# Kernel optimization log

Hardware: AMD Instinct MI355X
Metric: run time of the kernel (lower is better)

## Reference

```python
import jax, jax.numpy as jnp
import numpy as np

B, L, C, S, W, R = 2, 32, 32, 64, 64, 32
MH = 32  # forcing MLP hidden


def _conv3d(x, w, b, pad_hw):
    # x: [B, Cin, L, S, W], w: [Cout, Cin, 1, kh, kw]
    y = jax.lax.conv_general_dilated(
        x, w, window_strides=(1, 1, 1),
        padding=[(0, 0), (pad_hw, pad_hw), (pad_hw, pad_hw)],
        dimension_numbers=('NCDHW', 'OIDHW', 'NCDHW'))
    return y + b[None, :, None, None, None]


def _forward(x, listT, params_log_base, dispersion_mod, fm_W1, fm_b1, fm_W2, fm_b2,
             forcing_scale, U_re, U_im, V_re, V_im, pW_re, pW_im, pb_re, pb_im,
             convr_w, convr_b, convi_w, convi_b, projc_w, projc_b, ln_w, ln_b):
    b, l, c, s, w = x.shape
    r = U_re.shape[-1]
    pad = s // 4
    dt = listT.reshape(b, l, 1, 1, 1)

    # FFT with mirror padding along S
    xp = jnp.pad(x, ((0, 0), (0, 0), (0, 0), (pad, pad), (0, 0)), mode='reflect')
    h = jnp.fft.fft2(xp.astype(jnp.complex64), axes=(-2, -1), norm='ortho')

    # complex channel projection
    proj_W = pW_re + 1j * pW_im
    h = jnp.einsum('blcsw,cd->bldsw', h, proj_W)
    h = h + (pb_re + 1j * pb_im)[None, None, :, None, None]

    # back to spatial, crop pad, re-FFT
    hs = jnp.fft.ifft2(h, axes=(-2, -1), norm='ortho')[..., pad:-pad, :]
    h = jnp.fft.fft2(hs, axes=(-2, -1), norm='ortho')

    U = U_re + 1j * U_im          # [C, S, R]
    V = V_re + 1j * V_im          # [C, W, R]
    # zq[b,l,c,r,q] = sum_{s,w} h * conj(U)[c,s,r] * V[c,w,q]
    zq = jnp.einsum('blcsw,csr,cwq->blcrq', h, jnp.conj(U), V)

    nu_base = jnp.exp(params_log_base[0] + dispersion_mod[0]).reshape(1, 1, c, r, 1)
    th_base = jnp.exp(params_log_base[1] + dispersion_mod[1]).reshape(1, 1, c, r, 1)

    # forcing modulation
    ctx = x.mean(axis=(-2, -1))                       # [B, L, C]
    inp = jnp.concatenate([ctx, dt.reshape(b, l, 1)], axis=-1)
    mid = jnp.tanh(inp @ fm_W1 + fm_b1)
    mod = (mid @ fm_W2 + fm_b2).reshape(b, l, c, r, 2)
    dnu = (forcing_scale * jnp.tanh(mod[..., 0]))[..., None]
    dth = (forcing_scale * jnp.tanh(mod[..., 1]))[..., None]

    nu_t = jnp.maximum(nu_base * dt + dnu, 1e-6)       # [B, L, C, R, 1]
    th_t = th_base * dt + dth
    lamb = jnp.exp(jax.lax.complex(-nu_t, th_t))       # complex [B, L, C, R, 1]

    gamma = jnp.sqrt(jnp.maximum(1.0 - jnp.exp(-2.0 * nu_t), 1e-12))
    x_in = zq * gamma.astype(zq.dtype)                 # [B, L, C, R, R]

    # parallel linear-recurrence scan: z_t = lamb_t * z_{t-1} + x_t
    def comb(a, bb):
        a1, x1 = a
        a2, x2 = bb
        return a1 * a2, a2 * x1 + x2
    _, z_out = jax.lax.associative_scan(comb, (lamb, x_in), axis=1)

    # reconstruct spectral field and inverse FFT
    h_rec = jnp.einsum('blcrq,cwq,csr->blcsw', z_out, jnp.conj(V), U)
    h_sp = jnp.fft.ifft2(h_rec, axes=(-2, -1), norm='ortho')

    xr = jnp.transpose(h_sp.real, (0, 2, 1, 3, 4))     # [B, C, L, S, W]
    xi = jnp.transpose(h_sp.imag, (0, 2, 1, 3, 4))
    hr = _conv3d(xr, convr_w, convr_b, 1)
    hi = _conv3d(xi, convi_w, convi_b, 1)
    hf = _conv3d(jnp.concatenate([hr, hi], axis=1), projc_w, projc_b, 0)
    hf = jnp.transpose(hf, (0, 2, 1, 3, 4))            # [B, L, C, S, W]

    # LayerNorm over [S, W]
    mu = hf.mean(axis=(-2, -1), keepdims=True)
    var = hf.var(axis=(-2, -1), keepdims=True)
    hf = (hf - mu) / jnp.sqrt(var + 1e-5) * ln_w + ln_b

    return x + hf


def setup_inputs() -> dict:
    key = jax.random.key(0)
    ks = jax.random.split(key, 20)
    f32 = jnp.float32
    x = jax.random.normal(ks[0], (B, L, C, S, W), dtype=f32)
    listT = jax.random.uniform(ks[1], (B, L), dtype=f32, minval=0.5, maxval=1.5)

    r_min, r_max = 0.8, 0.99
    u1 = jax.random.uniform(ks[2], (C, R), dtype=f32)
    u2 = jax.random.uniform(ks[3], (C, R), dtype=f32)
    nu_log = jnp.log(-0.5 * jnp.log(u1 * (r_max ** 2 - r_min ** 2) + r_min ** 2))
    theta_log = jnp.log(u2 * (2.0 * np.pi))
    params_log_base = jnp.stack([nu_log, theta_log], axis=0)
    dispersion_mod = jnp.zeros((2, C, R), dtype=f32)

    fm_W1 = jax.random.normal(ks[4], (C + 1, MH), dtype=f32) / np.sqrt(C + 1)
    fm_b1 = jnp.zeros((MH,), dtype=f32)
    fm_W2 = jax.random.normal(ks[5], (MH, C * R * 2), dtype=f32) / np.sqrt(MH)
    fm_b2 = jnp.zeros((C * R * 2,), dtype=f32)
    forcing_scale = jnp.float32(0.1)

    cplx_scale = 1.0 / np.sqrt(2.0)
    U_re = jax.random.normal(ks[6], (C, S, R), dtype=f32) * cplx_scale / np.sqrt(S)
    U_im = jax.random.normal(ks[7], (C, S, R), dtype=f32) * cplx_scale / np.sqrt(S)
    V_re = jax.random.normal(ks[8], (C, W, R), dtype=f32) * cplx_scale / np.sqrt(W)
    V_im = jax.random.normal(ks[9], (C, W, R), dtype=f32) * cplx_scale / np.sqrt(W)
    pW_re = jax.random.normal(ks[10], (C, C), dtype=f32) * cplx_scale / np.sqrt(C)
    pW_im = jax.random.normal(ks[11], (C, C), dtype=f32) * cplx_scale / np.sqrt(C)
    pb_re = jnp.zeros((C,), dtype=f32)
    pb_im = jnp.zeros((C,), dtype=f32)

    convr_w = jax.random.normal(ks[12], (C, C, 1, 3, 3), dtype=f32) * (1.0 / np.sqrt(C * 9))
    convr_b = jnp.zeros((C,), dtype=f32)
    convi_w = jax.random.normal(ks[13], (C, C, 1, 3, 3), dtype=f32) * (1.0 / np.sqrt(C * 9))
    convi_b = jnp.zeros((C,), dtype=f32)
    projc_w = jax.random.normal(ks[14], (C, 2 * C, 1, 1, 1), dtype=f32) * (1.0 / np.sqrt(2 * C))
    projc_b = jnp.zeros((C,), dtype=f32)

    ln_w = jnp.ones((S, W), dtype=f32)
    ln_b = jnp.zeros((S, W), dtype=f32)

    return dict(x=x, listT=listT, params_log_base=params_log_base,
                dispersion_mod=dispersion_mod, fm_W1=fm_W1, fm_b1=fm_b1,
                fm_W2=fm_W2, fm_b2=fm_b2, forcing_scale=forcing_scale,
                U_re=U_re, U_im=U_im, V_re=V_re, V_im=V_im,
                pW_re=pW_re, pW_im=pW_im, pb_re=pb_re, pb_im=pb_im,
                convr_w=convr_w, convr_b=convr_b, convi_w=convi_w, convi_b=convi_b,
                projc_w=projc_w, projc_b=projc_b, ln_w=ln_w, ln_b=ln_b)


def reference(x, listT, params_log_base, dispersion_mod, fm_W1, fm_b1, fm_W2, fm_b2,
              forcing_scale, U_re, U_im, V_re, V_im, pW_re, pW_im, pb_re, pb_im,
              convr_w, convr_b, convi_w, convi_b, projc_w, projc_b, ln_w, ln_b):
    return _forward(x, listT, params_log_base, dispersion_mod, fm_W1, fm_b1, fm_W2,
                    fm_b2, forcing_scale, U_re, U_im, V_re, V_im, pW_re, pW_im,
                    pb_re, pb_im, convr_w, convr_b, convi_w, convi_b, projc_w,
                    projc_b, ln_w, ln_b)
```

## Files before the change

kernel.cpp:

```cpp
#include <hip/hip_runtime.h>


typedef __attribute__((ext_vector_type(8))) short short8;
typedef __attribute__((ext_vector_type(4))) float floatx4;

__device__ __forceinline__ unsigned pack_bf16(float re, float im) {
  unsigned a = __float_as_uint(re), b = __float_as_uint(im);
  a = (a + 0x7FFFu + ((a >> 16) & 1u)) >> 16;
  b = (b + 0x7FFFu + ((b >> 16) & 1u)) >> 16;
  return a | (b << 16);
}

__global__ __launch_bounds__(256) void k_prep(
    const float* __restrict__ U_re, const float* __restrict__ U_im,
    const float* __restrict__ V_re, const float* __restrict__ V_im,
    const float* __restrict__ projc_w,
    const float* __restrict__ convr_w, const float* __restrict__ convi_w,
    const float* __restrict__ x,
    unsigned* __restrict__ zqA, unsigned* __restrict__ recA,
    unsigned* __restrict__ recB, unsigned* __restrict__ Wtb,
    float* __restrict__ ctx) {
  const int bid = blockIdx.x;
  const int tid = threadIdx.x;
  if (bid < 2048) {
    __shared__ float2 tw[64];
    if (tid < 64) {
      float sa, ca;
      sincosf((float)tid * 0.09817477042468103f, &sa, &ca);
      tw[tid] = make_float2(ca, sa);
    }
    __syncthreads();
    int gid = bid * 256 + tid;
    const float *Ar, *Ai;
    int knum, mode, variant;
    bool plus;
    unsigned* dst;
    int didx;
    if (gid < 262144) {
      int c = gid >> 13, mat = (gid >> 11) & 3, m = (gid >> 6) & 31,
          kw = gid & 63;
      knum = kw; mode = m;
      if (mat < 2) { Ar = V_re + c * 2048; Ai = V_im + c * 2048; plus = false; }
      else         { Ar = U_re + c * 2048; Ai = U_im + c * 2048; plus = true; }
      variant = mat; dst = zqA; didx = gid;
    } else {
      int rid = gid - 262144;
      int c = rid >> 13, sub = rid & 8191;
      int which = sub >> 11, mm = (sub >> 5) & 63, k2 = sub & 31;
      knum = mm; mode = k2;
      if (which < 2) {
        Ar = U_re + c * 2048; Ai = U_im + c * 2048; plus = true;
        variant = 4 + which; dst = recA;
        didx = ((c * 2 + which) * 64 + mm) * 32 + k2;
      } else {
        Ar = V_re + c * 2048; Ai = V_im + c * 2048; plus = false;
        variant = 4 + which; dst = recB;
        didx = ((c * 2 + which - 2) * 64 + mm) * 32 + k2;
      }
    }
    float sr = 0.f, si = 0.f;
    for (int n = 0; n < 64; ++n) {
      float2 w = tw[(knum * n) & 63];
      float ar = Ar[n * 32 + mode], ai = Ai[n * 32 + mode];
      if (plus) { sr += ar * w.x - ai * w.y; si += ar * w.y + ai * w.x; }
      else      { sr += ar * w.x + ai * w.y; si += ai * w.x - ar * w.y; }
    }
    sr *= 0.125f; si *= 0.125f;
    unsigned pv;
    switch (variant) {
      case 0: pv = pack_bf16(sr, -si); break;
      case 1: pv = pack_bf16(si, sr); break;
      case 2: pv = pack_bf16(sr, si); break;
      case 3: pv = pack_bf16(-si, sr); break;
      case 4: pv = pack_bf16(sr, -si); break;
      case 5: pv = pack_bf16(si, sr); break;
      case 6: pv = pack_bf16(sr, si); break;
      default: pv = pack_bf16(-si, sr); break;
    }
    dst[didx] = pv;
  } else if (bid < 2084) {
    int gid = (bid - 2048) * 256 + tid;
    if (gid < 9216) {
      int co = gid / 288;
      int r2 = gid - co * 288;
      int tap = r2 >> 5, ci = r2 & 31;
      float sr = 0.f, si = 0.f;
      for (int m = 0; m < 32; ++m) {
        sr += projc_w[co * 64 + m]      * convr_w[(m * 32 + ci) * 9 + tap];
        si += projc_w[co * 64 + 32 + m] * convi_w[(m * 32 + ci) * 9 + tap];
      }
      Wtb[gid] = pack_bf16(sr, si);
    }
  } else {
    int blc = bid - 2084;
    const float* p = x + (size_t)blc * 4096;
    float s = 0.f;
    for (int i = tid; i < 4096; i += 256) s += p[i];
    for (int o = 32; o > 0; o >>= 1) s += __shfl_down(s, o, 64);
    __shared__ float wsum[4];
    if ((tid & 63) == 0) wsum[tid >> 6] = s;
    __syncthreads();
    if (tid == 0)
      ctx[blc] = (wsum[0] + wsum[1] + wsum[2] + wsum[3]) * (1.f / 4096.f);
  }
}

__global__ __launch_bounds__(256) void k_mix_mlp(
    const float* __restrict__ x, const float* __restrict__ pWr,
    const float* __restrict__ pWi, unsigned* __restrict__ hs,
    const float* __restrict__ ctx, const float* __restrict__ listT,
    const float* __restrict__ plb, const float* __restrict__ dmod,
    const float* __restrict__ W1, const float* __restrict__ b1,
    const float* __restrict__ W2, const float* __restrict__ b2,
    const float* __restrict__ fscale,
    float2* __restrict__ lam, float* __restrict__ gam) {
  const int tid = threadIdx.x;
  if (blockIdx.x < 1024) {
    int bl = blockIdx.x >> 4;
    int p = ((blockIdx.x & 15) << 8) + tid;
    const float* xb = x + (size_t)bl * 32 * 4096 + p;
    float xv[32];
#pragma unroll
    for (int ci = 0; ci < 32; ++ci) xv[ci] = xb[ci * 4096];
    unsigned* ho = hs + (size_t)bl * 32 * 4096 + p;
    for (int d = 0; d < 32; ++d) {
      float ar = 0.f, ai = 0.f;
#pragma unroll
      for (int ci = 0; ci < 32; ++ci) {
        float xc = xv[ci];
        ar += xc * pWr[ci * 32 + d];
        ai += xc * pWi[ci * 32 + d];
      }
      ho[(size_t)d * 4096] = pack_bf16(ar, ai);
    }
  } else {
    int bl = blockIdx.x - 1024;
    float dt = listT[bl];
    __shared__ float mid_s[32];
    if (tid < 32) {
      float a = b1[tid];
      for (int j = 0; j < 32; ++j) a += ctx[bl * 32 + j] * W1[j * 32 + tid];
      a += dt * W1[1024 + tid];
      mid_s[tid] = tanhf(a);
    }
    __syncthreads();
    float fs = fscale[0];
#pragma unroll
    for (int u = 0; u < 4; ++u) {
      int cr = u * 256 + tid;
      int col = cr * 2;
      float m0 = b2[col], m1 = b2[col + 1];
      for (int h = 0; h < 32; ++h) {
        float mh = mid_s[h];
        float2 w2 = *(const float2*)&W2[h * 2048 + col];
        m0 += mh * w2.x;
        m1 += mh * w2.y;
      }
      float dnu = fs * tanhf(m0);
      float dth = fs * tanhf(m1);
      float nub = expf(plb[cr] + dmod[cr]);
      float thb = expf(plb[1024 + cr] + dmod[1024 + cr]);
      float nut = fmaxf(nub * dt + dnu, 1e-6f);
      float tht = thb * dt + dth;
      float e = expf(-nut);
      float sa, ca;
      sincosf(tht, &sa, &ca);
      float g = sqrtf(fmaxf(1.f - expf(-2.f * nut), 1e-12f));
      int o = bl * 1024 + cr;
      lam[o] = make_float2(e * ca, e * sa);
      gam[o] = g;
    }
  }
}

__global__ __launch_bounds__(256) void k_zq(const unsigned* __restrict__ hs,
                                            const short* __restrict__ zqA,
                                            float2* __restrict__ zq) {
  __shared__ unsigned HsB[4096];
  __shared__ unsigned T2[2048];
  const int blc = blockIdx.x;
  const int c = blc & 31;
  const int tid = threadIdx.x;
  const int lane = tid & 63, wv = tid >> 6;
  const int qd = lane >> 4, ln = lane & 15;
  const int mt = wv >> 1, nth = wv & 1;
  {
    const uint4* hp = (const uint4*)(hs + (size_t)blc * 4096);
#pragma unroll
    for (int it = 0; it < 4; ++it) {
      int i4 = tid + it * 256;
      uint4 v = hp[i4];
      int s = i4 >> 4, w4 = i4 & 15;
      *(uint4*)&HsB[s * 64 + ((w4 ^ (s & 15)) << 2)] = v;
    }
  }
  const short* zA = zqA + (size_t)c * 4 * 32 * 128;
  short8 a1[4], a2[4], a3[4], a4[4];
#pragma unroll
  for (int t = 0; t < 4; ++t) {
    int row = mt * 16 + ln;
    a1[t] = *(const short8*)(zA + (0 * 32 + row) * 128 + t * 32 + qd * 8);
    a2[t] = *(const short8*)(zA + (1 * 32 + row) * 128 + t * 32 + qd * 8);
    a3[t] = *(const short8*)(zA + (2 * 32 + row) * 128 + t * 32 + qd * 8);
    a4[t] = *(const short8*)(zA + (3 * 32 + row) * 128 + t * 32 + qd * 8);
  }
  __syncthreads();
#pragma unroll
  for (int nti = 0; nti < 2; ++nti) {
    int nt = nth * 2 + nti;
    int n = nt * 16 + ln;
    floatx4 accr = {0.f, 0.f, 0.f, 0.f}, acci = {0.f, 0.f, 0.f, 0.f};
#pragma unroll
    for (int t = 0; t < 4; ++t) {
      short8 b = *(const short8*)&HsB[n * 64 + (((4 * t + qd) ^ (n & 15)) << 2)];
      accr = __builtin_amdgcn_mfma_f32_16x16x32_bf16(a1[t], b, accr, 0, 0, 0);
      acci = __builtin_amdgcn_mfma_f32_16x16x32_bf16(a2[t], b, acci, 0, 0, 0);
    }
#pragma unroll
    for (int j = 0; j < 4; ++j) {
      int q = mt * 16 + qd * 4 + j;
      int s = n;
      T2[q * 64 + (((s >> 2) ^ (q & 15)) << 2) + (s & 3)] = pack_bf16(accr[j], acci[j]);
    }
  }
  __syncthreads();
  {
    const int mt2 = wv >> 1, nt2 = wv & 1;
    int n = nt2 * 16 + ln;
    floatx4 zr = {0.f, 0.f, 0.f, 0.f}, zi = {0.f, 0.f, 0.f, 0.f};
#pragma unroll
    for (int t = 0; t < 4; ++t) {
      short8 b = *(const short8*)&T2[n * 64 + (((4 * t + qd) ^ (n & 15)) << 2)];
      zr = __builtin_amdgcn_mfma_f32_16x16x32_bf16(a3[t], b, zr, 0, 0, 0);
      zi = __builtin_amdgcn_mfma_f32_16x16x32_bf16(a4[t], b, zi, 0, 0, 0);
    }
    float2* zo = zq + (size_t)blc * 1024;
#pragma unroll
    for (int j = 0; j < 4; ++j) {
      int r = mt2 * 16 + qd * 4 + j;
      zo[r * 32 + n] = make_float2(zr[j], zi[j]);
    }
  }
}

__global__ __launch_bounds__(256) void k_scan(const float2* __restrict__ lam,
                                              const float* __restrict__ gam,
                                              const float2* __restrict__ zin,
                                              float2* __restrict__ zout) {
  int idx = blockIdx.x * 256 + threadIdx.x;
  int b = idx >> 15;
  int rem = idx & 32767;
  int c = rem >> 10;
  int r = (rem >> 5) & 31;
  int q = rem & 31;
  float zr = 0.f, zi = 0.f;
#pragma unroll 4
  for (int t = 0; t < 32; ++t) {
    int ocr = ((b * 32 + t) * 32 + c) * 32 + r;
    float2 lm = lam[ocr];
    float g = gam[ocr];
    size_t zidx = (size_t)ocr * 32 + q;
    float2 v = zin[zidx];
    float nr = lm.x * zr - lm.y * zi + g * v.x;
    float ni = lm.x * zi + lm.y * zr + g * v.y;
    zr = nr; zi = ni;
    zout[zidx] = make_float2(zr, zi);
  }
}

__global__ __launch_bounds__(256) void k_rec(const float2* __restrict__ zs,
                                             const short* __restrict__ recA,
                                             const short* __restrict__ recB,
                                             unsigned* __restrict__ hsp) {
  __shared__ unsigned zB[1024];
  __shared__ unsigned P[2048];
  const int blc = blockIdx.x;
  const int c = blc & 31;
  const int tid = threadIdx.x;
  const int lane = tid & 63, wv = tid >> 6;
  const int qd = lane >> 4, ln = lane & 15;
  {
    const float2* zp = zs + (size_t)blc * 1024;
#pragma unroll
    for (int it = 0; it < 4; ++it) {
      int i = tid + it * 256;
      float2 v = zp[i];
      int r = i >> 5, q = i & 31;
      zB[q * 32 + (((r >> 2) ^ (q & 7)) << 2) + (r & 3)] = pack_bf16(v.x, v.y);
    }
  }
  const short* rA = recA + (size_t)c * 2 * 64 * 64;
  short8 a5[2], a6[2];
#pragma unroll
  for (int t = 0; t < 2; ++t) {
    int row = wv * 16 + ln;
    a5[t] = *(const short8*)(rA + (0 * 64 + row) * 64 + t * 32 + qd * 8);
    a6[t] = *(const short8*)(rA + (1 * 64 + row) * 64 + t * 32 + qd * 8);
  }
  __syncthreads();
#pragma unroll
  for (int nt = 0; nt < 2; ++nt) {
    int n = nt * 16 + ln;
    floatx4 pr = {0.f, 0.f, 0.f, 0.f}, pi = {0.f, 0.f, 0.f, 0.f};
#pragma unroll
    for (int t = 0; t < 2; ++t) {
      short8 b = *(const short8*)&zB[n * 32 + (((4 * t + qd) ^ (n & 7)) << 2)];
      pr = __builtin_amdgcn_mfma_f32_16x16x32_bf16(a5[t], b, pr, 0, 0, 0);
      pi = __builtin_amdgcn_mfma_f32_16x16x32_bf16(a6[t], b, pi, 0, 0, 0);
    }
#pragma unroll
    for (int j = 0; j < 4; ++j) {
      int s = wv * 16 + qd * 4 + j;
      int q = n;
      P[s * 32 + (((q >> 2) ^ (s & 7)) << 2) + (q & 3)] = pack_bf16(pr[j], pi[j]);
    }
  }
  __syncthreads();
  const short* rB = recB + (size_t)c * 2 * 64 * 64;
  short8 pa[2];
#pragma unroll
  for (int t = 0; t < 2; ++t) {
    int row = wv * 16 + ln;
    pa[t] = *(const short8*)&P[row * 32 + (((4 * t + qd) ^ (row & 7)) << 2)];
  }
#pragma unroll
  for (int nt = 0; nt < 4; ++nt) {
    int n = nt * 16 + ln;
    floatx4 hr = {0.f, 0.f, 0.f, 0.f}, hi = {0.f, 0.f, 0.f, 0.f};
#pragma unroll
    for (int t = 0; t < 2; ++t) {
      short8 b5 = *(const short8*)(rB + (0 * 64 + n) * 64 + t * 32 + qd * 8);
      short8 b6 = *(const short8*)(rB + (1 * 64 + n) * 64 + t * 32 + qd * 8);
      hr = __builtin_amdgcn_mfma_f32_16x16x32_bf16(pa[t], b5, hr, 0, 0, 0);
      hi = __builtin_amdgcn_mfma_f32_16x16x32_bf16(pa[t], b6, hi, 0, 0, 0);
    }
    unsigned* ho = hsp + (size_t)blc * 4096;
#pragma unroll
    for (int j = 0; j < 4; ++j) {
      int s = wv * 16 + qd * 4 + j;
      ho[s * 64 + n] = pack_bf16(hr[j], hi[j]);
    }
  }
}

__global__ __launch_bounds__(256, 3) void k_conv(
    const unsigned* __restrict__ hsp, const short* __restrict__ Wtb,
    float* __restrict__ convout, float2* __restrict__ stats) {
  __shared__ unsigned lds_in[6 * 66 * 32];
  const int bl = blockIdx.x >> 4;
  const int slab = blockIdx.x & 15;
  const int y0 = slab * 4;
  const int tid = threadIdx.x;
  for (int i = tid; i < 384; i += 256) {
    int ci = i & 31, j = i >> 5;
    int yi = j >> 1, xi = (j & 1) ? 65 : 0;
    int slot = (ci >> 2) ^ (xi & 7);
    lds_in[(yi * 66 + xi) * 32 + slot * 4 + (ci & 3)] = 0u;
  }
#pragma unroll
  for (int t = 0; t < 12; ++t) {
    int i = t * 256 + tid;
    int ci = i & 31;
    int j = i >> 5;
    int yi = j >> 4, x4 = j & 15;
    int y = y0 + yi - 1;
    uint4 v = make_uint4(0u, 0u, 0u, 0u);
    if ((unsigned)y < 64u)
      v = *(const uint4*)(hsp + (((size_t)bl * 32 + ci) * 64 + y) * 64 + x4 * 4);
    int xb = 1 + x4 * 4;
#pragma unroll
    for (int jj = 0; jj < 4; ++jj) {
      int xi = xb + jj;
      int slot = (ci >> 2) ^ (xi & 7);
      lds_in[(yi * 66 + xi) * 32 + slot * 4 + (ci & 3)] =
          ((const unsigned*)&v)[jj];
    }
  }
  const int lane = tid & 63;
  const int wv = tid >> 6;
  const int co_t = wv >> 1;
  const int co = co_t * 16 + (lane & 15);
  const int qd = lane >> 4;
  short8 bfrag[18];
  {
    const short* wp = Wtb + (co * 9) * 64 + qd * 8;
#pragma unroll
    for (int tap = 0; tap < 9; ++tap)
#pragma unroll
      for (int kk = 0; kk < 2; ++kk)
        bfrag[tap * 2 + kk] = *(const short8*)(wp + tap * 64 + kk * 32);
  }
  __syncthreads();
  float ssum = 0.f, ssum2 = 0.f;
  const int xl = lane & 15;
  for (int m8 = 0; m8 < 8; ++m8) {
    int mt = (wv & 1) * 8 + m8;
    int ry = mt >> 2;
    int x0 = (mt & 3) * 16;
    floatx4 acc = {0.f, 0.f, 0.f, 0.f};
#pragma unroll
    for (int tap = 0; tap < 9; ++tap) {
      int dy = tap / 3, dx = tap - dy * 3;
      int yi = ry + dy;
      int xi = x0 + xl + dx;
#pragma unroll
      for (int kk = 0; kk < 2; ++kk) {
        int slot = ((kk << 2) | qd) ^ (xi & 7);
        const short8 a =
            *(const short8*)&lds_in[(yi * 66 + xi) * 32 + slot * 4];
        acc = __builtin_amdgcn_mfma_f32_16x16x32_bf16(a, bfrag[tap * 2 + kk],
                                                      acc, 0, 0, 0);
      }
    }
    size_t go = (((size_t)bl * 32 + co) * 64 + (y0 + ry)) * 64 + x0 + qd * 4;
    *(float4*)(convout + go) = make_float4(acc[0], acc[1], acc[2], acc[3]);
    ssum  += acc[0] + acc[1] + acc[2] + acc[3];
    ssum2 += acc[0] * acc[0] + acc[1] * acc[1] + acc[2] * acc[2] + acc[3] * acc[3];
  }
  ssum  += __shfl_down(ssum, 32, 64);
  ssum2 += __shfl_down(ssum2, 32, 64);
  ssum  += __shfl_down(ssum, 16, 64);
  ssum2 += __shfl_down(ssum2, 16, 64);
  if (lane < 16)
    stats[((size_t)bl * 32 + co_t * 16 + lane) * 32 + slab * 2 + (wv & 1)] =
        make_float2(ssum, ssum2);
}

__global__ __launch_bounds__(256) void k_ln(
    const float* __restrict__ convout, const float2* __restrict__ stats,
    const float* __restrict__ x, const float* __restrict__ ln_w,
    const float* __restrict__ ln_b, float* __restrict__ out) {
  const int blc = blockIdx.x;
  const int tid = threadIdx.x;
  __shared__ float sh_mu, sh_rs;
  if (tid < 64) {
    float2 v = (tid < 32) ? stats[(size_t)blc * 32 + tid] : make_float2(0.f, 0.f);
    float s = v.x, s2 = v.y;
#pragma unroll
    for (int o = 16; o > 0; o >>= 1) {
      s += __shfl_down(s, o, 64);
      s2 += __shfl_down(s2, o, 64);
    }
    if (tid == 0) {
      float mu = s * (1.f / 4096.f);
      float var = s2 * (1.f / 4096.f) - mu * mu;
      sh_mu = mu;
      sh_rs = rsqrtf(var + 1e-5f);
    }
  }
  __syncthreads();
  float mu = sh_mu, rs = sh_rs;
  const float4* cp = (const float4*)(convout + (size_t)blc * 4096);
  const float4* xp = (const float4*)(x + (size_t)blc * 4096);
  const float4* lwp = (const float4*)ln_w;
  const float4* lbp = (const float4*)ln_b;
  float4* op = (float4*)(out + (size_t)blc * 4096);
#pragma unroll
  for (int k = 0; k < 4; ++k) {
    int i = tid + k * 256;
    float4 cv = cp[i], xv = xp[i], lw = lwp[i], lb = lbp[i];
    float4 o;
    o.x = xv.x + (cv.x - mu) * rs * lw.x + lb.x;
    o.y = xv.y + (cv.y - mu) * rs * lw.y + lb.y;
    o.z = xv.z + (cv.z - mu) * rs * lw.z + lb.z;
    o.w = xv.w + (cv.w - mu) * rs * lw.w + lb.w;
    op[i] = o;
  }
}

extern "C" void kernel_launch(void* const* d_in, const int* in_sizes, int n_in,
                              void* d_out, int out_size, void* d_ws,
                              size_t ws_size, hipStream_t stream) {
  const float* x       = (const float*)d_in[0];
  const float* listT   = (const float*)d_in[1];
  const float* plb     = (const float*)d_in[2];
  const float* dmod    = (const float*)d_in[3];
  const float* fm_W1   = (const float*)d_in[4];
  const float* fm_b1   = (const float*)d_in[5];
  const float* fm_W2   = (const float*)d_in[6];
  const float* fm_b2   = (const float*)d_in[7];
  const float* fscale  = (const float*)d_in[8];
  const float* U_re    = (const float*)d_in[9];
  const float* U_im    = (const float*)d_in[10];
  const float* V_re    = (const float*)d_in[11];
  const float* V_im    = (const float*)d_in[12];
  const float* pW_re   = (const float*)d_in[13];
  const float* pW_im   = (const float*)d_in[14];
  const float* convr_w = (const float*)d_in[17];
  const float* convi_w = (const float*)d_in[19];
  const float* projc_w = (const float*)d_in[21];
  const float* ln_w    = (const float*)d_in[23];
  const float* ln_b    = (const float*)d_in[24];
  float* out = (float*)d_out;

  float* wsf = (float*)d_ws;
  unsigned* hs  = (unsigned*)wsf;
  unsigned* hsp = (unsigned*)wsf;
  float*    convout = wsf + 8388608;
  unsigned* zqAp  = (unsigned*)(wsf + 8388608);
  unsigned* recAp = (unsigned*)(wsf + 8388608 + 262144);
  unsigned* recBp = (unsigned*)(wsf + 8388608 + 393216);
  float2*   zq  = (float2*)(wsf + 16777216);
  size_t off = 16777216 + 4194304;
  float2* zs = (float2*)(wsf + off);
  size_t need_with_zs = (size_t)(off + 4194304 + 470016) * 4;
  bool sep = ws_size >= need_with_zs;
  if (sep) off += 4194304; else zs = zq;
  float2*   lam  = (float2*)(wsf + off);
  float2*   stats = lam;
  float*    gam  = wsf + off + 131072;
  float*    ctx  = wsf + off + 458752;
  unsigned* Wtb  = (unsigned*)(wsf + off + 460800);

  k_prep<<<4132, 256, 0, stream>>>(U_re, U_im, V_re, V_im, projc_w,
                                   convr_w, convi_w, x, zqAp, recAp, recBp,
                                   Wtb, ctx);
  k_mix_mlp<<<1088, 256, 0, stream>>>(x, pW_re, pW_im, hs, ctx, listT, plb,
                                      dmod, fm_W1, fm_b1, fm_W2, fm_b2,
                                      fscale, lam, gam);
  k_zq<<<2048, 256, 0, stream>>>(hs, (const short*)zqAp, zq);
  k_scan<<<256, 256, 0, stream>>>(lam, gam, zq, zs);
  k_rec<<<2048, 256, 0, stream>>>(zs, (const short*)recAp, (const short*)recBp, hsp);
  k_conv<<<1024, 256, 0, stream>>>(hsp, (const short*)Wtb, convout, stats);
  k_ln<<<2048, 256, 0, stream>>>(convout, stats, x, ln_w, ln_b, out);
}
```

Before: 277.0 us.

## Use MFMA for channel mix, prefetch scan, bf16 conv output, rework conv tiling

The channel projection moves from scalar FMA loops to bf16 MFMA, with x staged as packed bf16 in swizzled LDS. The scan kernel now runs one block per (b,c) with coalesced loads and software prefetch of the next timestep. The conv kernel has each wave compute both 16-channel halves over its own x-strip, stores its output as bf16 and writes stats to a separate buffer with 64 partials per channel. k_ln reads the bf16 conv output. These changes target ALU and memory traffic, at the cost of extra bf16 rounding, lower occupancy in k_conv, and only 64 blocks in k_scan.

```diff
diff --git a/kernel.cpp b/kernel.cpp
--- a/kernel.cpp
+++ b/kernel.cpp
@@ -9,6 +9,10 @@
   a = (a + 0x7FFFu + ((a >> 16) & 1u)) >> 16;
   b = (b + 0x7FFFu + ((b >> 16) & 1u)) >> 16;
   return a | (b << 16);
+}
+__device__ __forceinline__ unsigned short bf16r(float v) {
+  unsigned a = __float_as_uint(v);
+  return (unsigned short)((a + 0x7FFFu + ((a >> 16) & 1u)) >> 16);
 }
 
 __global__ __launch_bounds__(256) void k_prep(
@@ -114,29 +118,60 @@
     const float* __restrict__ W2, const float* __restrict__ b2,
     const float* __restrict__ fscale,
     float2* __restrict__ lam, float* __restrict__ gam) {
-  const int tid = threadIdx.x;
-  if (blockIdx.x < 1024) {
-    int bl = blockIdx.x >> 4;
-    int p = ((blockIdx.x & 15) << 8) + tid;
-    const float* xb = x + (size_t)bl * 32 * 4096 + p;
-    float xv[32];
-#pragma unroll
-    for (int ci = 0; ci < 32; ++ci) xv[ci] = xb[ci * 4096];
-    unsigned* ho = hs + (size_t)bl * 32 * 4096 + p;
-    for (int d = 0; d < 32; ++d) {
-      float ar = 0.f, ai = 0.f;
-#pragma unroll
-      for (int ci = 0; ci < 32; ++ci) {
-        float xc = xv[ci];
-        ar += xc * pWr[ci * 32 + d];
-        ai += xc * pWi[ci * 32 + d];
-      }
-      ho[(size_t)d * 4096] = pack_bf16(ar, ai);
+  __shared__ unsigned xb_s[512 * 20];
+  __shared__ float mid_s[32];
+  const int tid = threadIdx.x;
+  if (blockIdx.x < 512) {
+    const int bl = blockIdx.x >> 3;
+    const int pxbase = (blockIdx.x & 7) * 512;
+    const float* xb = x + (size_t)bl * 131072 + pxbase;
+#pragma unroll
+    for (int t = 0; t < 8; ++t) {
+      int i = t * 256 + tid;
+      int c2 = i & 15, g4 = i >> 4;
+      float4 a = *(const float4*)(xb + (2 * c2) * 4096 + g4 * 4);
+      float4 b = *(const float4*)(xb + (2 * c2 + 1) * 4096 + g4 * 4);
+#pragma unroll
+      for (int j = 0; j < 4; ++j) {
+        int px = g4 * 4 + j;
+        xb_s[px * 20 + (((c2 >> 2) ^ (px & 3)) << 2) + (c2 & 3)] =
+            pack_bf16(((const float*)&a)[j], ((const float*)&b)[j]);
+      }
+    }
+    const int lane = tid & 63, wv = tid >> 6;
+    const int qd = lane >> 4, ln = lane & 15;
+    short8 arL, aiL, arH, aiH;
+#pragma unroll
+    for (int j = 0; j < 8; ++j) {
+      int ci = qd * 8 + j;
+      ((short*)&arL)[j] = (short)bf16r(pWr[ci * 32 + ln]);
+      ((short*)&aiL)[j] = (short)bf16r(pWi[ci * 32 + ln]);
+      ((short*)&arH)[j] = (short)bf16r(pWr[ci * 32 + 16 + ln]);
+      ((short*)&aiH)[j] = (short)bf16r(pWi[ci * 32 + 16 + ln]);
+    }
+    __syncthreads();
+#pragma unroll
+    for (int pt = 0; pt < 8; ++pt) {
+      int pxt = wv * 8 + pt;
+      int pxl = pxt * 16 + ln;
+      short8 bfr =
+          *(const short8*)&xb_s[pxl * 20 + ((qd ^ (pxl & 3)) << 2)];
+      floatx4 dRL = {0.f, 0.f, 0.f, 0.f}, dIL = {0.f, 0.f, 0.f, 0.f};
+      floatx4 dRH = {0.f, 0.f, 0.f, 0.f}, dIH = {0.f, 0.f, 0.f, 0.f};
+      dRL = __builtin_amdgcn_mfma_f32_16x16x32_bf16(arL, bfr, dRL, 0, 0, 0);
+      dIL = __builtin_amdgcn_mfma_f32_16x16x32_bf16(aiL, bfr, dIL, 0, 0, 0);
+      dRH = __builtin_amdgcn_mfma_f32_16x16x32_bf16(arH, bfr, dRH, 0, 0, 0);
+      dIH = __builtin_amdgcn_mfma_f32_16x16x32_bf16(aiH, bfr, dIH, 0, 0, 0);
+      unsigned* ho = hs + (size_t)bl * 131072 + pxbase + pxt * 16 + ln;
+#pragma unroll
+      for (int j = 0; j < 4; ++j) {
+        ho[(qd * 4 + j) * 4096] = pack_bf16(dRL[j], dIL[j]);
+        ho[(16 + qd * 4 + j) * 4096] = pack_bf16(dRH[j], dIH[j]);
+      }
     }
   } else {
-    int bl = blockIdx.x - 1024;
+    int bl = blockIdx.x - 512;
     float dt = listT[bl];
-    __shared__ float mid_s[32];
     if (tid < 32) {
       float a = b1[tid];
       for (int j = 0; j < 32; ++j) a += ctx[bl * 32 + j] * W1[j * 32 + tid];
@@ -245,26 +280,48 @@
 
 __global__ __launch_bounds__(256) void k_scan(const float2* __restrict__ lam,
                                               const float* __restrict__ gam,
-                                              const float2* __restrict__ zin,
-                                              float2* __restrict__ zout) {
-  int idx = blockIdx.x * 256 + threadIdx.x;
-  int b = idx >> 15;
-  int rem = idx & 32767;
-  int c = rem >> 10;
-  int r = (rem >> 5) & 31;
-  int q = rem & 31;
-  float zr = 0.f, zi = 0.f;
-#pragma unroll 4
+                                              const float2* zin,
+                                              float2* zout) {
+  const int b = blockIdx.x >> 5, c = blockIdx.x & 31;
+  const int tid = threadIdx.x;
+  float2 st[4] = {{0.f, 0.f}, {0.f, 0.f}, {0.f, 0.f}, {0.f, 0.f}};
+  float2 v[4], lmv[4];
+  float gv[4];
+  {
+    size_t zb = ((size_t)(b * 32) * 32 + c) * 1024;
+    int pb = (b * 32) * 1024 + c * 32;
+#pragma unroll
+    for (int j = 0; j < 4; ++j) {
+      int rq = tid + 256 * j;
+      v[j] = zin[zb + rq];
+      lmv[j] = lam[pb + (rq >> 5)];
+      gv[j] = gam[pb + (rq >> 5)];
+    }
+  }
   for (int t = 0; t < 32; ++t) {
-    int ocr = ((b * 32 + t) * 32 + c) * 32 + r;
-    float2 lm = lam[ocr];
-    float g = gam[ocr];
-    size_t zidx = (size_t)ocr * 32 + q;
-    float2 v = zin[zidx];
-    float nr = lm.x * zr - lm.y * zi + g * v.x;
-    float ni = lm.x * zi + lm.y * zr + g * v.y;
-    zr = nr; zi = ni;
-    zout[zidx] = make_float2(zr, zi);
+    float2 nv[4], nlm[4];
+    float ng[4];
+    if (t < 31) {
+      size_t zb = ((size_t)(b * 32 + t + 1) * 32 + c) * 1024;
+      int pb = (b * 32 + t + 1) * 1024 + c * 32;
+#pragma unroll
+      for (int j = 0; j < 4; ++j) {
+        int rq = tid + 256 * j;
+        nv[j] = zin[zb + rq];
+        nlm[j] = lam[pb + (rq >> 5)];
+        ng[j] = gam[pb + (rq >> 5)];
+      }
+    }
+    size_t zb = ((size_t)(b * 32 + t) * 32 + c) * 1024;
+#pragma unroll
+    for (int j = 0; j < 4; ++j) {
+      float nr = lmv[j].x * st[j].x - lmv[j].y * st[j].y + gv[j] * v[j].x;
+      float ni = lmv[j].x * st[j].y + lmv[j].y * st[j].x + gv[j] * v[j].y;
+      st[j] = make_float2(nr, ni);
+      zout[zb + tid + 256 * j] = st[j];
+    }
+#pragma unroll
+    for (int j = 0; j < 4; ++j) { v[j] = nv[j]; lmv[j] = nlm[j]; gv[j] = ng[j]; }
   }
 }
 
@@ -343,9 +400,9 @@
   }
 }
 
-__global__ __launch_bounds__(256, 3) void k_conv(
+__global__ __launch_bounds__(256, 2) void k_conv(
     const unsigned* __restrict__ hsp, const short* __restrict__ Wtb,
-    float* __restrict__ convout, float2* __restrict__ stats) {
+    unsigned short* __restrict__ convout, float2* __restrict__ stats) {
   __shared__ unsigned lds_in[6 * 66 * 32];
   const int bl = blockIdx.x >> 4;
   const int slab = blockIdx.x & 15;
@@ -378,26 +435,26 @@
   }
   const int lane = tid & 63;
   const int wv = tid >> 6;
-  const int co_t = wv >> 1;
-  const int co = co_t * 16 + (lane & 15);
+  const int co = lane & 15;
   const int qd = lane >> 4;
-  short8 bfrag[18];
+  short8 bL[18], bH[18];
   {
-    const short* wp = Wtb + (co * 9) * 64 + qd * 8;
+    const short* wpL = Wtb + (co * 9) * 64 + qd * 8;
+    const short* wpH = Wtb + ((co + 16) * 9) * 64 + qd * 8;
 #pragma unroll
     for (int tap = 0; tap < 9; ++tap)
 #pragma unroll
-      for (int kk = 0; kk < 2; ++kk)
-        bfrag[tap * 2 + kk] = *(const short8*)(wp + tap * 64 + kk * 32);
+      for (int kk = 0; kk < 2; ++kk) {
+        bL[tap * 2 + kk] = *(const short8*)(wpL + tap * 64 + kk * 32);
+        bH[tap * 2 + kk] = *(const short8*)(wpH + tap * 64 + kk * 32);
+      }
   }
   __syncthreads();
-  float ssum = 0.f, ssum2 = 0.f;
+  float sL = 0.f, s2L = 0.f, sH = 0.f, s2H = 0.f;
+  const int x0 = wv * 16;
   const int xl = lane & 15;
-  for (int m8 = 0; m8 < 8; ++m8) {
-    int mt = (wv & 1) * 8 + m8;
-    int ry = mt >> 2;
-    int x0 = (mt & 3) * 16;
-    floatx4 acc = {0.f, 0.f, 0.f, 0.f};
+  for (int ry = 0; ry < 4; ++ry) {
+    floatx4 aL = {0.f, 0.f, 0.f, 0.f}, aH = {0.f, 0.f, 0.f, 0.f};
 #pragma unroll
     for (int tap = 0; tap < 9; ++tap) {
       int dy = tap / 3, dx = tap - dy * 3;
@@ -408,36 +465,46 @@
         int slot = ((kk << 2) | qd) ^ (xi & 7);
         const short8 a =
             *(const short8*)&lds_in[(yi * 66 + xi) * 32 + slot * 4];
-        acc = __builtin_amdgcn_mfma_f32_16x16x32_bf16(a, bfrag[tap * 2 + kk],
-                                                      acc, 0, 0, 0);
-      }
-    }
-    size_t go = (((size_t)bl * 32 + co) * 64 + (y0 + ry)) * 64 + x0 + qd * 4;
-    *(float4*)(convout + go) = make_float4(acc[0], acc[1], acc[2], acc[3]);
-    ssum  += acc[0] + acc[1] + acc[2] + acc[3];
-    ssum2 += acc[0] * acc[0] + acc[1] * acc[1] + acc[2] * acc[2] + acc[3] * acc[3];
-  }
-  ssum  += __shfl_down(ssum, 32, 64);
-  ssum2 += __shfl_down(ssum2, 32, 64);
-  ssum  += __shfl_down(ssum, 16, 64);
-  ssum2 += __shfl_down(ssum2, 16, 64);
-  if (lane < 16)
-    stats[((size_t)bl * 32 + co_t * 16 + lane) * 32 + slab * 2 + (wv & 1)] =
-        make_float2(ssum, ssum2);
+        aL = __builtin_amdgcn_mfma_f32_16x16x32_bf16(a, bL[tap * 2 + kk], aL, 0, 0, 0);
+        aH = __builtin_amdgcn_mfma_f32_16x16x32_bf16(a, bH[tap * 2 + kk], aH, 0, 0, 0);
+      }
+    }
+    size_t goL = (((size_t)bl * 32 + co) * 64 + (y0 + ry)) * 64 + x0 + qd * 4;
+    size_t goH = goL + (size_t)16 * 4096;
+    *(uint2*)(convout + goL) =
+        make_uint2(pack_bf16(aL[0], aL[1]), pack_bf16(aL[2], aL[3]));
+    *(uint2*)(convout + goH) =
+        make_uint2(pack_bf16(aH[0], aH[1]), pack_bf16(aH[2], aH[3]));
+#pragma unroll
+    for (int j = 0; j < 4; ++j) {
+      sL += aL[j]; s2L += aL[j] * aL[j];
+      sH += aH[j]; s2H += aH[j] * aH[j];
+    }
+  }
+  sL += __shfl_down(sL, 32, 64);  s2L += __shfl_down(s2L, 32, 64);
+  sH += __shfl_down(sH, 32, 64);  s2H += __shfl_down(s2H, 32, 64);
+  sL += __shfl_down(sL, 16, 64);  s2L += __shfl_down(s2L, 16, 64);
+  sH += __shfl_down(sH, 16, 64);  s2H += __shfl_down(s2H, 16, 64);
+  if (lane < 16) {
+    stats[((size_t)bl * 32 + lane) * 64 + slab * 4 + wv] = make_float2(sL, s2L);
+    stats[((size_t)bl * 32 + 16 + lane) * 64 + slab * 4 + wv] =
+        make_float2(sH, s2H);
+  }
 }
 
 __global__ __launch_bounds__(256) void k_ln(
-    const float* __restrict__ convout, const float2* __restrict__ stats,
-    const float* __restrict__ x, const float* __restrict__ ln_w,
-    const float* __restrict__ ln_b, float* __restrict__ out) {
+    const unsigned short* __restrict__ convout,
+    const float2* __restrict__ stats, const float* __restrict__ x,
+    const float* __restrict__ ln_w, const float* __restrict__ ln_b,
+    float* __restrict__ out) {
   const int blc = blockIdx.x;
   const int tid = threadIdx.x;
   __shared__ float sh_mu, sh_rs;
   if (tid < 64) {
-    float2 v = (tid < 32) ? stats[(size_t)blc * 32 + tid] : make_float2(0.f, 0.f);
+    float2 v = stats[(size_t)blc * 64 + tid];
     float s = v.x, s2 = v.y;
 #pragma unroll
-    for (int o = 16; o > 0; o >>= 1) {
+    for (int o = 32; o > 0; o >>= 1) {
       s += __shfl_down(s, o, 64);
       s2 += __shfl_down(s2, o, 64);
     }
@@ -450,7 +517,7 @@
   }
   __syncthreads();
   float mu = sh_mu, rs = sh_rs;
-  const float4* cp = (const float4*)(convout + (size_t)blc * 4096);
+  const uint2* cp = (const uint2*)(convout + (size_t)blc * 4096);
   const float4* xp = (const float4*)(x + (size_t)blc * 4096);
   const float4* lwp = (const float4*)ln_w;
   const float4* lbp = (const float4*)ln_b;
@@ -458,12 +525,17 @@
 #pragma unroll
   for (int k = 0; k < 4; ++k) {
     int i = tid + k * 256;
-    float4 cv = cp[i], xv = xp[i], lw = lwp[i], lb = lbp[i];
+    uint2 cv = cp[i];
+    float4 xv = xp[i], lw = lwp[i], lb = lbp[i];
+    float c0 = __uint_as_float(cv.x << 16);
+    float c1 = __uint_as_float(cv.x & 0xFFFF0000u);
+    float c2 = __uint_as_float(cv.y << 16);
+    float c3 = __uint_as_float(cv.y & 0xFFFF0000u);
     float4 o;
-    o.x = xv.x + (cv.x - mu) * rs * lw.x + lb.x;
-    o.y = xv.y + (cv.y - mu) * rs * lw.y + lb.y;
-    o.z = xv.z + (cv.z - mu) * rs * lw.z + lb.z;
-    o.w = xv.w + (cv.w - mu) * rs * lw.w + lb.w;
+    o.x = xv.x + (c0 - mu) * rs * lw.x + lb.x;
+    o.y = xv.y + (c1 - mu) * rs * lw.y + lb.y;
+    o.z = xv.z + (c2 - mu) * rs * lw.z + lb.z;
+    o.w = xv.w + (c3 - mu) * rs * lw.w + lb.w;
     op[i] = o;
   }
 }
@@ -496,10 +568,11 @@
   float* wsf = (float*)d_ws;
   unsigned* hs  = (unsigned*)wsf;
   unsigned* hsp = (unsigned*)wsf;
-  float*    convout = wsf + 8388608;
   unsigned* zqAp  = (unsigned*)(wsf + 8388608);
   unsigned* recAp = (unsigned*)(wsf + 8388608 + 262144);
   unsigned* recBp = (unsigned*)(wsf + 8388608 + 393216);
+  unsigned short* convout = (unsigned short*)(wsf + 8388608);
+  float2*   stats = (float2*)(wsf + 12582912);
   float2*   zq  = (float2*)(wsf + 16777216);
   size_t off = 16777216 + 4194304;
   float2* zs = (float2*)(wsf + off);
@@ -507,7 +580,6 @@
   bool sep = ws_size >= need_with_zs;
   if (sep) off += 4194304; else zs = zq;
   float2*   lam  = (float2*)(wsf + off);
-  float2*   stats = lam;
   float*    gam  = wsf + off + 131072;
   float*    ctx  = wsf + off + 458752;
   unsigned* Wtb  = (unsigned*)(wsf + off + 460800);
@@ -515,11 +587,11 @@
   k_prep<<<4132, 256, 0, stream>>>(U_re, U_im, V_re, V_im, projc_w,
                                    convr_w, convi_w, x, zqAp, recAp, recBp,
                                    Wtb, ctx);
-  k_mix_mlp<<<1088, 256, 0, stream>>>(x, pW_re, pW_im, hs, ctx, listT, plb,
-                                      dmod, fm_W1, fm_b1, fm_W2, fm_b2,
-                                      fscale, lam, gam);
+  k_mix_mlp<<<576, 256, 0, stream>>>(x, pW_re, pW_im, hs, ctx, listT, plb,
+                                     dmod, fm_W1, fm_b1, fm_W2, fm_b2,
+                                     fscale, lam, gam);
   k_zq<<<2048, 256, 0, stream>>>(hs, (const short*)zqAp, zq);
-  k_scan<<<256, 256, 0, stream>>>(lam, gam, zq, zs);
+  k_scan<<<64, 256, 0, stream>>>(lam, gam, zq, zs);
   k_rec<<<2048, 256, 0, stream>>>(zs, (const short*)recAp, (const short*)recBp, hsp);
   k_conv<<<1024, 256, 0, stream>>>(hsp, (const short*)Wtb, convout, stats);
   k_ln<<<2048, 256, 0, stream>>>(convout, stats, x, ln_w, ln_b, out);
```

New measurement: 258.8 us. 1.07x faster.
